# Optimization experiments

Measured on AMD Instinct MI355X. Metric: run time of the kernel, lower is better.

## Reference

```python
import jax, jax.numpy as jnp
import numpy as np

B, T, C, COND, H = 64, 4096, 64, 512, 256
SCALE_EPS = 1e-6
LOGSCALE_FACTOR = 3.0  # glow LinearZeros convention
LEAK = 0.01            # torch LeakyReLU default slope


def setup_inputs() -> dict:
    key = jax.random.key(0)
    ks = jax.random.split(key, 10)
    perm = jnp.asarray(np.random.RandomState(0).permutation(C), dtype=jnp.int32)
    return {
        "input_seq": jax.random.normal(ks[0], (B, T, C), jnp.float32),
        "speech_cond": jax.random.normal(ks[1], (B, T, COND), jnp.float32),
        "actnorm_bias": 0.1 * jax.random.normal(ks[2], (C,), jnp.float32),
        "actnorm_logs": 0.1 * jax.random.normal(ks[3], (C,), jnp.float32),
        "perm": perm,
        "W1": jax.random.normal(ks[4], (C // 2 + COND, H), jnp.float32) / np.sqrt(C // 2 + COND),
        "b1": 0.01 * jax.random.normal(ks[5], (H,), jnp.float32),
        "W2": 0.05 * jax.random.normal(ks[6], (H, C), jnp.float32) / np.sqrt(H),
        "b2": 0.01 * jax.random.normal(ks[7], (C,), jnp.float32),
        "logs2": 0.05 * jax.random.normal(ks[8], (C,), jnp.float32),
    }


def reference(input_seq, speech_cond, actnorm_bias, actnorm_logs, perm, W1, b1, W2, b2, logs2):
    # The torch module loops over timesteps, but each step is independent
    # (no RNN state is used), so we batch all timesteps at once.
    # --- ActNorm2d (per-channel affine); pixels=1 per timestep ---
    z = (input_seq + actnorm_bias) * jnp.exp(actnorm_logs)          # [B,T,C]
    logdet = jnp.full((B,), T * jnp.sum(actnorm_logs))              # [B]
    # --- Permute2d (fixed shuffle of channels) ---
    z = z[..., perm]
    # --- split coupling ---
    z1, z2 = z[..., : C // 2], z[..., C // 2 :]                     # [B,T,C/2] each
    # f_seq: Linear + LeakyReLU (dropout off at eval) + LinearZeros
    h = jnp.concatenate([z1, speech_cond], axis=-1)                 # [B,T,C/2+COND]
    h = jax.nn.leaky_relu(jnp.einsum("btk,kh->bth", h, W1) + b1, LEAK)
    h = (jnp.einsum("bth,hc->btc", h, W2) + b2) * jnp.exp(logs2 * LOGSCALE_FACTOR)  # [B,T,C]
    # --- affine transform: split 'cross' (interleaved) ---
    shift = h[..., 0::2]
    scale = jnp.maximum(jax.nn.sigmoid(h[..., 1::2] + 2.0), SCALE_EPS)
    z2 = (z2 + shift) * scale
    logdet = logdet + jnp.sum(jnp.log(scale), axis=(1, 2))          # [B]
    z_seq = jnp.concatenate([z1, z2], axis=-1)                      # [B,T,C]
    return z_seq, logdet
```

## Files before the change

### kernel.cpp

```cpp
#include <hip/hip_runtime.h>
#include <stdint.h>

#define B_ 64
#define T_ 4096
#define C_ 64
#define COND_ 512
#define H_ 256

typedef __attribute__((ext_vector_type(8))) short short8;
typedef __attribute__((ext_vector_type(4))) float f32x4;
typedef __attribute__((ext_vector_type(2))) float f32x2;
typedef __attribute__((ext_vector_type(2))) unsigned int u32x2;

__device__ __forceinline__ unsigned short f2bf(float x) {
  union { float f; unsigned u; } v; v.f = x;
  unsigned r = v.u + 0x7FFFu + ((v.u >> 16) & 1u);
  return (unsigned short)(r >> 16);
}

__device__ __forceinline__ short8 cvt8(f32x4 lo, f32x4 hi) {
  short8 t;
  t[0] = (short)f2bf(lo[0]); t[1] = (short)f2bf(lo[1]);
  t[2] = (short)f2bf(lo[2]); t[3] = (short)f2bf(lo[3]);
  t[4] = (short)f2bf(hi[0]); t[5] = (short)f2bf(hi[1]);
  t[6] = (short)f2bf(hi[2]); t[7] = (short)f2bf(hi[3]);
  return t;
}

__device__ __forceinline__ void lgkm_barrier() {
  asm volatile("s_waitcnt lgkmcnt(0)" ::: "memory");
  __builtin_amdgcn_s_barrier();
}

#define WS_W1   0
#define WS_W2   278528
#define WS_PB   311296
#define WS_PS   311552
#define WS_B2S  311808

__global__ __launch_bounds__(256) void prep_kernel(
    const float* __restrict__ W1, const float* __restrict__ W2,
    const float* __restrict__ anb, const float* __restrict__ anl,
    const int* __restrict__ perm, const float* __restrict__ b2,
    const float* __restrict__ logs2,
    unsigned short* __restrict__ wsW1, unsigned short* __restrict__ wsW2,
    float* __restrict__ pb, float* __restrict__ ps, float* __restrict__ b2s,
    float* __restrict__ out_ld)
{
  int id = blockIdx.x * 256 + threadIdx.x;
  if (id < 544 * 256) {
    int feat = id & 255, k = id >> 8;
    int r = (k < 512) ? (k + 32) : (k - 512);
    float v = W1[r * 256 + feat];
    int s = k >> 5, MI = feat >> 4;
    int l = (feat & 15) + 16 * ((k >> 3) & 3), i = k & 7;
    wsW1[((s * 16 + MI) * 64 + l) * 8 + i] = f2bf(v);
  } else if (id < 544 * 256 + 256 * 64) {
    int id2 = id - 544 * 256;
    int ch = id2 & 63, k = id2 >> 6;
    float v = W2[k * 64 + ch] * expf(logs2[ch] * 3.0f);
    int s2 = k >> 5, MI2 = ch >> 4;
    int l = (ch & 15) + 16 * ((k >> 3) & 3), i = k & 7;
    wsW2[((s2 * 4 + MI2) * 64 + l) * 8 + i] = f2bf(v);
  } else {
    int c = id - (544 * 256 + 256 * 64);
    if (c < 64) {
      int p = perm[c];
      pb[c] = anb[p];
      ps[c] = expf(anl[p]);
    } else if (c < 128) {
      int ch = c - 64;
      b2s[ch] = b2[ch] * expf(logs2[ch] * 3.0f);
    } else if (c < 192) {
      int b = c - 128;
      float s = 0.f;
      for (int j = 0; j < 64; ++j) s += anl[j];
      out_ld[b] = (float)T_ * s;
    }
  }
}

__global__ __launch_bounds__(256) void flow_main(
    const float* __restrict__ input, const float* __restrict__ cond,
    const int* __restrict__ perm, const float* __restrict__ b1,
    const unsigned short* __restrict__ wsW1, const unsigned short* __restrict__ wsW2,
    const float* __restrict__ pb, const float* __restrict__ ps,
    const float* __restrict__ b2s,
    float* __restrict__ out, float* __restrict__ out_ld)
{
  __shared__ union SM {
    short lA[2][64 * 64];
    short lHT[64 * 256];
  } sm;

  const int tid = threadIdx.x;
  const int w  = tid >> 6;
  const int l  = tid & 63;
  const int lr = l & 15;
  const int lh = l >> 4;
  const long long m0 = (long long)blockIdx.x * 64;

  const int stok = tid >> 2;
  const int skc  = (tid & 3) * 16;
  const float* cpS = cond + (m0 + stok) * 512 + skc;

#define W1F(s, mi) (*(const short8*)&wsW1[((((s) * 16) + (4 * w + (mi))) * 64 + l) * 8])

  short8 aZ[4];
#pragma unroll
  for (int mi = 0; mi < 4; ++mi) aZ[mi] = W1F(16, mi);

  short8 afA[2][4], afB[2][4];
#pragma unroll
  for (int h = 0; h < 2; ++h)
#pragma unroll
    for (int mi = 0; mi < 4; ++mi) afA[h][mi] = W1F(h, mi);
  f32x4 sA0 = *(const f32x4*)(cpS);
  f32x4 sA1 = *(const f32x4*)(cpS + 4);
  f32x4 sA2 = *(const f32x4*)(cpS + 8);
  f32x4 sA3 = *(const f32x4*)(cpS + 12);

#pragma unroll
  for (int h = 0; h < 2; ++h)
#pragma unroll
    for (int mi = 0; mi < 4; ++mi) afB[h][mi] = W1F(2 + h, mi);
  f32x4 sB0 = *(const f32x4*)(cpS + 64);
  f32x4 sB1 = *(const f32x4*)(cpS + 68);
  f32x4 sB2 = *(const f32x4*)(cpS + 72);
  f32x4 sB3 = *(const f32x4*)(cpS + 76);

  {
    const int c0 = (tid & 3) * 8;
    const float* ip = input + (m0 + stok) * 64;
    short8 v;
#pragma unroll
    for (int j = 0; j < 8; ++j) {
      int c = c0 + j;
      v[j] = (short)f2bf((ip[perm[c]] + pb[c]) * ps[c]);
    }
    const int S = (tid & 3) ^ (stok & 7);
    *(short8*)&sm.lA[0][stok * 64 + S * 8] = v;
  }

  f32x4 acc[4][4];
#pragma unroll
  for (int mi = 0; mi < 4; ++mi)
#pragma unroll
    for (int nj = 0; nj < 4; ++nj)
      acc[mi][nj] = (f32x4)0.0f;

  lgkm_barrier();

  {
    short8 bz[4];
#pragma unroll
    for (int nj = 0; nj < 4; ++nj) {
      const int tok = 16 * nj + lr;
      bz[nj] = *(const short8*)&sm.lA[0][tok * 64 + ((lh ^ (tok & 7)) * 8)];
    }
#pragma unroll
    for (int mi = 0; mi < 4; ++mi)
#pragma unroll
      for (int nj = 0; nj < 4; ++nj)
        acc[mi][nj] = __builtin_amdgcn_mfma_f32_16x16x32_bf16(
            aZ[mi], bz[nj], acc[mi][nj], 0, 0, 0);

    short8 c0v = cvt8(sA0, sA1), c1v = cvt8(sA2, sA3);
    const int S0 = 2 * (tid & 3);
    *(short8*)&sm.lA[1][stok * 64 + ((S0 ^ (stok & 7)) * 8)] = c0v;
    *(short8*)&sm.lA[1][stok * 64 + (((S0 + 1) ^ (stok & 7)) * 8)] = c1v;
  }
  lgkm_barrier();

#pragma unroll 1
  for (int p = 0; p < 4; ++p) {
    {
      short8 bf0[4], bf1[4];
#pragma unroll
      for (int nj = 0; nj < 4; ++nj) {
        const int tok = 16 * nj + lr;
        bf0[nj] = *(const short8*)&sm.lA[1][tok * 64 + ((lh ^ (tok & 7)) * 8)];
        bf1[nj] = *(const short8*)&sm.lA[1][tok * 64 + (((4 + lh) ^ (tok & 7)) * 8)];
      }
#pragma unroll
      for (int mi = 0; mi < 4; ++mi)
#pragma unroll
        for (int nj = 0; nj < 4; ++nj)
          acc[mi][nj] = __builtin_amdgcn_mfma_f32_16x16x32_bf16(
              afA[0][mi], bf0[nj], acc[mi][nj], 0, 0, 0);
#pragma unroll
      for (int mi = 0; mi < 4; ++mi)
#pragma unroll
        for (int nj = 0; nj < 4; ++nj)
          acc[mi][nj] = __builtin_amdgcn_mfma_f32_16x16x32_bf16(
              afA[1][mi], bf1[nj], acc[mi][nj], 0, 0, 0);
    }
    if (p <= 2) {
#pragma unroll
      for (int h = 0; h < 2; ++h)
#pragma unroll
        for (int mi = 0; mi < 4; ++mi) afA[h][mi] = W1F(4 * p + 4 + h, mi);
      const float* cp = cpS + (2 * p + 2) * 64;
      sA0 = *(const f32x4*)(cp);
      sA1 = *(const f32x4*)(cp + 4);
      sA2 = *(const f32x4*)(cp + 8);
      sA3 = *(const f32x4*)(cp + 12);
    }
    {
      short8 c0v = cvt8(sB0, sB1), c1v = cvt8(sB2, sB3);
      const int S0 = 2 * (tid & 3);
      *(short8*)&sm.lA[0][stok * 64 + ((S0 ^ (stok & 7)) * 8)] = c0v;
      *(short8*)&sm.lA[0][stok * 64 + (((S0 + 1) ^ (stok & 7)) * 8)] = c1v;
    }
    lgkm_barrier();

    {
      short8 bf0[4], bf1[4];
#pragma unroll
      for (int nj = 0; nj < 4; ++nj) {
        const int tok = 16 * nj + lr;
        bf0[nj] = *(const short8*)&sm.lA[0][tok * 64 + ((lh ^ (tok & 7)) * 8)];
        bf1[nj] = *(const short8*)&sm.lA[0][tok * 64 + (((4 + lh) ^ (tok & 7)) * 8)];
      }
#pragma unroll
      for (int mi = 0; mi < 4; ++mi)
#pragma unroll
        for (int nj = 0; nj < 4; ++nj)
          acc[mi][nj] = __builtin_amdgcn_mfma_f32_16x16x32_bf16(
              afB[0][mi], bf0[nj], acc[mi][nj], 0, 0, 0);
#pragma unroll
      for (int mi = 0; mi < 4; ++mi)
#pragma unroll
        for (int nj = 0; nj < 4; ++nj)
          acc[mi][nj] = __builtin_amdgcn_mfma_f32_16x16x32_bf16(
              afB[1][mi], bf1[nj], acc[mi][nj], 0, 0, 0);
    }
    if (p <= 2) {
#pragma unroll
      for (int h = 0; h < 2; ++h)
#pragma unroll
        for (int mi = 0; mi < 4; ++mi) afB[h][mi] = W1F(4 * p + 6 + h, mi);
      const float* cp = cpS + (2 * p + 3) * 64;
      sB0 = *(const f32x4*)(cp);
      sB1 = *(const f32x4*)(cp + 4);
      sB2 = *(const f32x4*)(cp + 8);
      sB3 = *(const f32x4*)(cp + 12);
    }
    if (p <= 2) {
      short8 c0v = cvt8(sA0, sA1), c1v = cvt8(sA2, sA3);
      const int S0 = 2 * (tid & 3);
      *(short8*)&sm.lA[1][stok * 64 + ((S0 ^ (stok & 7)) * 8)] = c0v;
      *(short8*)&sm.lA[1][stok * 64 + (((S0 + 1) ^ (stok & 7)) * 8)] = c1v;
    }
    lgkm_barrier();
  }

#pragma unroll
  for (int mi = 0; mi < 4; ++mi) {
    const int f0 = 64 * w + 16 * mi + 4 * lh;
    const f32x4 b1v = *(const f32x4*)&b1[f0];
#pragma unroll
    for (int nj = 0; nj < 4; ++nj) {
      const int tok = 16 * nj + lr;
      f32x4 v = acc[mi][nj];
      float h0 = v[0] + b1v[0]; h0 = h0 > 0.f ? h0 : 0.01f * h0;
      float h1 = v[1] + b1v[1]; h1 = h1 > 0.f ? h1 : 0.01f * h1;
      float h2 = v[2] + b1v[2]; h2 = h2 > 0.f ? h2 : 0.01f * h2;
      float h3 = v[3] + b1v[3]; h3 = h3 > 0.f ? h3 : 0.01f * h3;
      u32x2 pk;
      pk[0] = (unsigned)f2bf(h0) | ((unsigned)f2bf(h1) << 16);
      pk[1] = (unsigned)f2bf(h2) | ((unsigned)f2bf(h3) << 16);
      const int off = (tok * 512 + f0 * 2) ^ ((tok & 7) << 4);
      *(u32x2*)((char*)sm.lHT + off) = pk;
    }
  }

  short8 a2r[8];
#pragma unroll
  for (int s2 = 0; s2 < 8; ++s2)
    a2r[s2] = *(const short8*)&wsW2[((s2 * 4 + w) * 64 + l) * 8];

  lgkm_barrier();

  f32x4 acc2[4];
#pragma unroll
  for (int nj = 0; nj < 4; ++nj) acc2[nj] = (f32x4)0.0f;

#pragma unroll
  for (int s2 = 0; s2 < 8; ++s2) {
#pragma unroll
    for (int nj = 0; nj < 4; ++nj) {
      const int tok = 16 * nj + lr;
      const int off = (tok * 512 + (32 * s2 + 8 * lh) * 2) ^ ((tok & 7) << 4);
      const short8 hb = *(const short8*)((char*)sm.lHT + off);
      acc2[nj] = __builtin_amdgcn_mfma_f32_16x16x32_bf16(a2r[s2], hb, acc2[nj], 0, 0, 0);
    }
  }

  const int j0 = 8 * w + 2 * lh;
  const int pA = perm[j0],      pB = perm[j0 + 1];
  const int pC = perm[32 + j0], pD = perm[33 + j0];
  const float bA = pb[j0],      sA = ps[j0];
  const float bB = pb[j0 + 1],  sB = ps[j0 + 1];
  const float bC = pb[32 + j0], sC = ps[32 + j0];
  const float bD = pb[33 + j0], sD = ps[33 + j0];
  const f32x4 b2v = *(const f32x4*)&b2s[16 * w + 4 * lh];

  float ldp = 0.f;
#pragma unroll
  for (int nj = 0; nj < 4; ++nj) {
    const long long row = m0 + 16 * nj + lr;
    const float* ip = input + row * 64;
    float* op = out + row * 64;
    f32x4 v = acc2[nj];
    const float sh0 = v[0] + b2v[0];
    const float sc0 = v[1] + b2v[1];
    const float sh1 = v[2] + b2v[2];
    const float sc1 = v[3] + b2v[3];
    const float scl0 = fmaxf(1.f / (1.f + expf(-(sc0 + 2.f))), 1e-6f);
    const float scl1 = fmaxf(1.f / (1.f + expf(-(sc1 + 2.f))), 1e-6f);
    f32x2 z1o, z2o;
    z1o[0] = (ip[pA] + bA) * sA;
    z1o[1] = (ip[pB] + bB) * sB;
    z2o[0] = ((ip[pC] + bC) * sC + sh0) * scl0;
    z2o[1] = ((ip[pD] + bD) * sD + sh1) * scl1;
    *(f32x2*)(op + j0) = z1o;
    *(f32x2*)(op + 32 + j0) = z2o;
    ldp += logf(scl0) + logf(scl1);
  }

#pragma unroll
  for (int off = 32; off > 0; off >>= 1) ldp += __shfl_xor(ldp, off, 64);
  if (l == 0) atomicAdd(&out_ld[blockIdx.x >> 6], ldp);
}

extern "C" void kernel_launch(void* const* d_in, const int* in_sizes, int n_in,
                              void* d_out, int out_size, void* d_ws, size_t ws_size,
                              hipStream_t stream)
{
  const float* input = (const float*)d_in[0];
  const float* cond  = (const float*)d_in[1];
  const float* anb   = (const float*)d_in[2];
  const float* anl   = (const float*)d_in[3];
  const int*   perm  = (const int*)d_in[4];
  const float* W1    = (const float*)d_in[5];
  const float* b1    = (const float*)d_in[6];
  const float* W2    = (const float*)d_in[7];
  const float* b2    = (const float*)d_in[8];
  const float* logs2 = (const float*)d_in[9];

  float* out    = (float*)d_out;
  float* out_ld = out + (long long)B_ * T_ * C_;

  char* ws = (char*)d_ws;
  unsigned short* wsW1 = (unsigned short*)(ws + WS_W1);
  unsigned short* wsW2 = (unsigned short*)(ws + WS_W2);
  float* pbp  = (float*)(ws + WS_PB);
  float* psp  = (float*)(ws + WS_PS);
  float* b2sp = (float*)(ws + WS_B2S);

  prep_kernel<<<609, 256, 0, stream>>>(W1, W2, anb, anl, perm, b2, logs2,
                                       wsW1, wsW2, pbp, psp, b2sp, out_ld);
  flow_main<<<4096, 256, 0, stream>>>(input, cond, perm, b1, wsW1, wsW2,
                                      pbp, psp, b2sp, out, out_ld);
}
```

Measured before the change: 263.3 us.

## Make flow_main persistent with cross-tile prefetch of input and cond

Launches a fixed grid of 1024 blocks that loop over the 4096 token tiles in a grid-stride fashion, hoisting per-thread permutation and actnorm parameters out of the loop. While the second GEMM and epilogue of one tile run, the next tile's input and first cond slices are loaded into registers. The aim is to hide the global-load latency at tile start and to amortise setup work. The cost is higher register pressure and fewer resident blocks, which may reduce occupancy-based latency hiding. The log-determinant also changes from logf(a)+logf(b) to logf(a*b).

```diff
diff --git a/kernel.cpp b/kernel.cpp
--- a/kernel.cpp
+++ b/kernel.cpp
@@ -6,6 +6,8 @@
 #define C_ 64
 #define COND_ 512
 #define H_ 256
+#define NTILE 4096
+#define GRID_ 1024
 
 typedef __attribute__((ext_vector_type(8))) short short8;
 typedef __attribute__((ext_vector_type(4))) float f32x4;
@@ -98,240 +100,266 @@
   const int l  = tid & 63;
   const int lr = l & 15;
   const int lh = l >> 4;
-  const long long m0 = (long long)blockIdx.x * 64;
 
   const int stok = tid >> 2;
   const int skc  = (tid & 3) * 16;
-  const float* cpS = cond + (m0 + stok) * 512 + skc;
+  const int c0   = (tid & 3) * 8;
 
 #define W1F(s, mi) (*(const short8*)&wsW1[((((s) * 16) + (4 * w + (mi))) * 64 + l) * 8])
 
-  short8 aZ[4];
-#pragma unroll
-  for (int mi = 0; mi < 4; ++mi) aZ[mi] = W1F(16, mi);
-
-  short8 afA[2][4], afB[2][4];
-#pragma unroll
-  for (int h = 0; h < 2; ++h)
-#pragma unroll
-    for (int mi = 0; mi < 4; ++mi) afA[h][mi] = W1F(h, mi);
-  f32x4 sA0 = *(const f32x4*)(cpS);
-  f32x4 sA1 = *(const f32x4*)(cpS + 4);
-  f32x4 sA2 = *(const f32x4*)(cpS + 8);
-  f32x4 sA3 = *(const f32x4*)(cpS + 12);
-
-#pragma unroll
-  for (int h = 0; h < 2; ++h)
-#pragma unroll
-    for (int mi = 0; mi < 4; ++mi) afB[h][mi] = W1F(2 + h, mi);
-  f32x4 sB0 = *(const f32x4*)(cpS + 64);
-  f32x4 sB1 = *(const f32x4*)(cpS + 68);
-  f32x4 sB2 = *(const f32x4*)(cpS + 72);
-  f32x4 sB3 = *(const f32x4*)(cpS + 76);
-
+  int   ipoff[8]; float pbz[8], psz[8];
+#pragma unroll
+  for (int j = 0; j < 8; ++j) {
+    int c = c0 + j;
+    ipoff[j] = perm[c];
+    pbz[j] = pb[c];
+    psz[j] = ps[c];
+  }
+  const int j0 = 8 * w + 2 * lh;
+  const int pi0 = perm[j0],      pi1 = perm[j0 + 1];
+  const int pi2 = perm[32 + j0], pi3 = perm[33 + j0];
+  const float eb0 = pb[j0],      es0 = ps[j0];
+  const float eb1 = pb[j0 + 1],  es1 = ps[j0 + 1];
+  const float eb2 = pb[32 + j0], es2 = ps[32 + j0];
+  const float eb3 = pb[33 + j0], es3 = ps[33 + j0];
+  const f32x4 b2v = *(const f32x4*)&b2s[16 * w + 4 * lh];
+
+  int tile = blockIdx.x;
+  float z1g[8];
+  f32x4 sA0, sA1, sA2, sA3, sB0, sB1, sB2, sB3;
   {
-    const int c0 = (tid & 3) * 8;
-    const float* ip = input + (m0 + stok) * 64;
-    short8 v;
-#pragma unroll
-    for (int j = 0; j < 8; ++j) {
-      int c = c0 + j;
-      v[j] = (short)f2bf((ip[perm[c]] + pb[c]) * ps[c]);
-    }
-    const int S = (tid & 3) ^ (stok & 7);
-    *(short8*)&sm.lA[0][stok * 64 + S * 8] = v;
+    const float* ipn = input + ((long long)tile * 64 + stok) * 64;
+#pragma unroll
+    for (int j = 0; j < 8; ++j) z1g[j] = ipn[ipoff[j]];
+    const float* cpn = cond + ((long long)tile * 64 + stok) * 512 + skc;
+    sA0 = *(const f32x4*)(cpn);      sA1 = *(const f32x4*)(cpn + 4);
+    sA2 = *(const f32x4*)(cpn + 8);  sA3 = *(const f32x4*)(cpn + 12);
+    sB0 = *(const f32x4*)(cpn + 64); sB1 = *(const f32x4*)(cpn + 68);
+    sB2 = *(const f32x4*)(cpn + 72); sB3 = *(const f32x4*)(cpn + 76);
   }
 
-  f32x4 acc[4][4];
-#pragma unroll
-  for (int mi = 0; mi < 4; ++mi)
-#pragma unroll
-    for (int nj = 0; nj < 4; ++nj)
-      acc[mi][nj] = (f32x4)0.0f;
-
-  lgkm_barrier();
-
-  {
-    short8 bz[4];
-#pragma unroll
-    for (int nj = 0; nj < 4; ++nj) {
-      const int tok = 16 * nj + lr;
-      bz[nj] = *(const short8*)&sm.lA[0][tok * 64 + ((lh ^ (tok & 7)) * 8)];
-    }
+#pragma unroll 1
+  for (; tile < NTILE; tile += GRID_) {
+    const long long m0 = (long long)tile * 64;
+    const float* cpS = cond + (m0 + stok) * 512 + skc;
+
+    short8 aZ[4], afA[2][4], afB[2][4];
+#pragma unroll
+    for (int mi = 0; mi < 4; ++mi) aZ[mi] = W1F(16, mi);
+#pragma unroll
+    for (int h = 0; h < 2; ++h)
+#pragma unroll
+      for (int mi = 0; mi < 4; ++mi) afA[h][mi] = W1F(h, mi);
+#pragma unroll
+    for (int h = 0; h < 2; ++h)
+#pragma unroll
+      for (int mi = 0; mi < 4; ++mi) afB[h][mi] = W1F(2 + h, mi);
+
+    lgkm_barrier();
+
+    {
+      short8 v;
+#pragma unroll
+      for (int j = 0; j < 8; ++j)
+        v[j] = (short)f2bf((z1g[j] + pbz[j]) * psz[j]);
+      const int S = (tid & 3) ^ (stok & 7);
+      *(short8*)&sm.lA[0][stok * 64 + S * 8] = v;
+    }
+
+    f32x4 acc[4][4];
 #pragma unroll
     for (int mi = 0; mi < 4; ++mi)
 #pragma unroll
       for (int nj = 0; nj < 4; ++nj)
-        acc[mi][nj] = __builtin_amdgcn_mfma_f32_16x16x32_bf16(
-            aZ[mi], bz[nj], acc[mi][nj], 0, 0, 0);
-
-    short8 c0v = cvt8(sA0, sA1), c1v = cvt8(sA2, sA3);
-    const int S0 = 2 * (tid & 3);
-    *(short8*)&sm.lA[1][stok * 64 + ((S0 ^ (stok & 7)) * 8)] = c0v;
-    *(short8*)&sm.lA[1][stok * 64 + (((S0 + 1) ^ (stok & 7)) * 8)] = c1v;
-  }
-  lgkm_barrier();
-
-#pragma unroll 1
-  for (int p = 0; p < 4; ++p) {
+        acc[mi][nj] = (f32x4)0.0f;
+
+    lgkm_barrier();
+
     {
-      short8 bf0[4], bf1[4];
+      short8 bz[4];
 #pragma unroll
       for (int nj = 0; nj < 4; ++nj) {
         const int tok = 16 * nj + lr;
-        bf0[nj] = *(const short8*)&sm.lA[1][tok * 64 + ((lh ^ (tok & 7)) * 8)];
-        bf1[nj] = *(const short8*)&sm.lA[1][tok * 64 + (((4 + lh) ^ (tok & 7)) * 8)];
+        bz[nj] = *(const short8*)&sm.lA[0][tok * 64 + ((lh ^ (tok & 7)) * 8)];
       }
 #pragma unroll
       for (int mi = 0; mi < 4; ++mi)
 #pragma unroll
         for (int nj = 0; nj < 4; ++nj)
           acc[mi][nj] = __builtin_amdgcn_mfma_f32_16x16x32_bf16(
-              afA[0][mi], bf0[nj], acc[mi][nj], 0, 0, 0);
-#pragma unroll
-      for (int mi = 0; mi < 4; ++mi)
-#pragma unroll
-        for (int nj = 0; nj < 4; ++nj)
-          acc[mi][nj] = __builtin_amdgcn_mfma_f32_16x16x32_bf16(
-              afA[1][mi], bf1[nj], acc[mi][nj], 0, 0, 0);
-    }
-    if (p <= 2) {
-#pragma unroll
-      for (int h = 0; h < 2; ++h)
-#pragma unroll
-        for (int mi = 0; mi < 4; ++mi) afA[h][mi] = W1F(4 * p + 4 + h, mi);
-      const float* cp = cpS + (2 * p + 2) * 64;
-      sA0 = *(const f32x4*)(cp);
-      sA1 = *(const f32x4*)(cp + 4);
-      sA2 = *(const f32x4*)(cp + 8);
-      sA3 = *(const f32x4*)(cp + 12);
-    }
-    {
-      short8 c0v = cvt8(sB0, sB1), c1v = cvt8(sB2, sB3);
-      const int S0 = 2 * (tid & 3);
-      *(short8*)&sm.lA[0][stok * 64 + ((S0 ^ (stok & 7)) * 8)] = c0v;
-      *(short8*)&sm.lA[0][stok * 64 + (((S0 + 1) ^ (stok & 7)) * 8)] = c1v;
-    }
-    lgkm_barrier();
-
-    {
-      short8 bf0[4], bf1[4];
-#pragma unroll
-      for (int nj = 0; nj < 4; ++nj) {
-        const int tok = 16 * nj + lr;
-        bf0[nj] = *(const short8*)&sm.lA[0][tok * 64 + ((lh ^ (tok & 7)) * 8)];
-        bf1[nj] = *(const short8*)&sm.lA[0][tok * 64 + (((4 + lh) ^ (tok & 7)) * 8)];
-      }
-#pragma unroll
-      for (int mi = 0; mi < 4; ++mi)
-#pragma unroll
-        for (int nj = 0; nj < 4; ++nj)
-          acc[mi][nj] = __builtin_amdgcn_mfma_f32_16x16x32_bf16(
-              afB[0][mi], bf0[nj], acc[mi][nj], 0, 0, 0);
-#pragma unroll
-      for (int mi = 0; mi < 4; ++mi)
-#pragma unroll
-        for (int nj = 0; nj < 4; ++nj)
-          acc[mi][nj] = __builtin_amdgcn_mfma_f32_16x16x32_bf16(
-              afB[1][mi], bf1[nj], acc[mi][nj], 0, 0, 0);
-    }
-    if (p <= 2) {
-#pragma unroll
-      for (int h = 0; h < 2; ++h)
-#pragma unroll
-        for (int mi = 0; mi < 4; ++mi) afB[h][mi] = W1F(4 * p + 6 + h, mi);
-      const float* cp = cpS + (2 * p + 3) * 64;
-      sB0 = *(const f32x4*)(cp);
-      sB1 = *(const f32x4*)(cp + 4);
-      sB2 = *(const f32x4*)(cp + 8);
-      sB3 = *(const f32x4*)(cp + 12);
-    }
-    if (p <= 2) {
+              aZ[mi], bz[nj], acc[mi][nj], 0, 0, 0);
+
       short8 c0v = cvt8(sA0, sA1), c1v = cvt8(sA2, sA3);
       const int S0 = 2 * (tid & 3);
       *(short8*)&sm.lA[1][stok * 64 + ((S0 ^ (stok & 7)) * 8)] = c0v;
       *(short8*)&sm.lA[1][stok * 64 + (((S0 + 1) ^ (stok & 7)) * 8)] = c1v;
     }
     lgkm_barrier();
+
+#pragma unroll 1
+    for (int p = 0; p < 4; ++p) {
+      {
+        short8 bf0[4], bf1[4];
+#pragma unroll
+        for (int nj = 0; nj < 4; ++nj) {
+          const int tok = 16 * nj + lr;
+          bf0[nj] = *(const short8*)&sm.lA[1][tok * 64 + ((lh ^ (tok & 7)) * 8)];
+          bf1[nj] = *(const short8*)&sm.lA[1][tok * 64 + (((4 + lh) ^ (tok & 7)) * 8)];
+        }
+#pragma unroll
+        for (int mi = 0; mi < 4; ++mi)
+#pragma unroll
+          for (int nj = 0; nj < 4; ++nj)
+            acc[mi][nj] = __builtin_amdgcn_mfma_f32_16x16x32_bf16(
+                afA[0][mi], bf0[nj], acc[mi][nj], 0, 0, 0);
+#pragma unroll
+        for (int mi = 0; mi < 4; ++mi)
+#pragma unroll
+          for (int nj = 0; nj < 4; ++nj)
+            acc[mi][nj] = __builtin_amdgcn_mfma_f32_16x16x32_bf16(
+                afA[1][mi], bf1[nj], acc[mi][nj], 0, 0, 0);
+      }
+      if (p <= 2) {
+#pragma unroll
+        for (int h = 0; h < 2; ++h)
+#pragma unroll
+          for (int mi = 0; mi < 4; ++mi) afA[h][mi] = W1F(4 * p + 4 + h, mi);
+        const float* cp = cpS + (2 * p + 2) * 64;
+        sA0 = *(const f32x4*)(cp);
+        sA1 = *(const f32x4*)(cp + 4);
+        sA2 = *(const f32x4*)(cp + 8);
+        sA3 = *(const f32x4*)(cp + 12);
+      }
+      {
+        short8 c0v = cvt8(sB0, sB1), c1v = cvt8(sB2, sB3);
+        const int S0 = 2 * (tid & 3);
+        *(short8*)&sm.lA[0][stok * 64 + ((S0 ^ (stok & 7)) * 8)] = c0v;
+        *(short8*)&sm.lA[0][stok * 64 + (((S0 + 1) ^ (stok & 7)) * 8)] = c1v;
+      }
+      lgkm_barrier();
+
+      {
+        short8 bf0[4], bf1[4];
+#pragma unroll
+        for (int nj = 0; nj < 4; ++nj) {
+          const int tok = 16 * nj + lr;
+          bf0[nj] = *(const short8*)&sm.lA[0][tok * 64 + ((lh ^ (tok & 7)) * 8)];
+          bf1[nj] = *(const short8*)&sm.lA[0][tok * 64 + (((4 + lh) ^ (tok & 7)) * 8)];
+        }
+#pragma unroll
+        for (int mi = 0; mi < 4; ++mi)
+#pragma unroll
+          for (int nj = 0; nj < 4; ++nj)
+            acc[mi][nj] = __builtin_amdgcn_mfma_f32_16x16x32_bf16(
+                afB[0][mi], bf0[nj], acc[mi][nj], 0, 0, 0);
+#pragma unroll
+        for (int mi = 0; mi < 4; ++mi)
+#pragma unroll
+          for (int nj = 0; nj < 4; ++nj)
+            acc[mi][nj] = __builtin_amdgcn_mfma_f32_16x16x32_bf16(
+                afB[1][mi], bf1[nj], acc[mi][nj], 0, 0, 0);
+      }
+      if (p <= 2) {
+#pragma unroll
+        for (int h = 0; h < 2; ++h)
+#pragma unroll
+          for (int mi = 0; mi < 4; ++mi) afB[h][mi] = W1F(4 * p + 6 + h, mi);
+        const float* cp = cpS + (2 * p + 3) * 64;
+        sB0 = *(const f32x4*)(cp);
+        sB1 = *(const f32x4*)(cp + 4);
+        sB2 = *(const f32x4*)(cp + 8);
+        sB3 = *(const f32x4*)(cp + 12);
+      }
+      if (p <= 2) {
+        short8 c0v = cvt8(sA0, sA1), c1v = cvt8(sA2, sA3);
+        const int S0 = 2 * (tid & 3);
+        *(short8*)&sm.lA[1][stok * 64 + ((S0 ^ (stok & 7)) * 8)] = c0v;
+        *(short8*)&sm.lA[1][stok * 64 + (((S0 + 1) ^ (stok & 7)) * 8)] = c1v;
+      }
+      lgkm_barrier();
+    }
+
+    short8 a2r[8];
+#pragma unroll
+    for (int s2 = 0; s2 < 8; ++s2)
+      a2r[s2] = *(const short8*)&wsW2[((s2 * 4 + w) * 64 + l) * 8];
+
+    const int ntile = tile + GRID_;
+    if (ntile < NTILE) {
+      const float* ipn = input + ((long long)ntile * 64 + stok) * 64;
+#pragma unroll
+      for (int j = 0; j < 8; ++j) z1g[j] = ipn[ipoff[j]];
+      const float* cpn = cond + ((long long)ntile * 64 + stok) * 512 + skc;
+      sA0 = *(const f32x4*)(cpn);      sA1 = *(const f32x4*)(cpn + 4);
+      sA2 = *(const f32x4*)(cpn + 8);  sA3 = *(const f32x4*)(cpn + 12);
+      sB0 = *(const f32x4*)(cpn + 64); sB1 = *(const f32x4*)(cpn + 68);
+      sB2 = *(const f32x4*)(cpn + 72); sB3 = *(const f32x4*)(cpn + 76);
+    }
+
+#pragma unroll
+    for (int mi = 0; mi < 4; ++mi) {
+      const int f0 = 64 * w + 16 * mi + 4 * lh;
+      const f32x4 b1v = *(const f32x4*)&b1[f0];
+#pragma unroll
+      for (int nj = 0; nj < 4; ++nj) {
+        const int tok = 16 * nj + lr;
+        f32x4 v = acc[mi][nj];
+        float h0 = v[0] + b1v[0]; h0 = h0 > 0.f ? h0 : 0.01f * h0;
+        float h1 = v[1] + b1v[1]; h1 = h1 > 0.f ? h1 : 0.01f * h1;
+        float h2 = v[2] + b1v[2]; h2 = h2 > 0.f ? h2 : 0.01f * h2;
+        float h3 = v[3] + b1v[3]; h3 = h3 > 0.f ? h3 : 0.01f * h3;
+        u32x2 pk;
+        pk[0] = (unsigned)f2bf(h0) | ((unsigned)f2bf(h1) << 16);
+        pk[1] = (unsigned)f2bf(h2) | ((unsigned)f2bf(h3) << 16);
+        const int off = (tok * 512 + f0 * 2) ^ ((tok & 7) << 4);
+        *(u32x2*)((char*)sm.lHT + off) = pk;
+      }
+    }
+
+    lgkm_barrier();
+
+    f32x4 acc2[4];
+#pragma unroll
+    for (int nj = 0; nj < 4; ++nj) acc2[nj] = (f32x4)0.0f;
+
+#pragma unroll
+    for (int s2 = 0; s2 < 8; ++s2) {
+#pragma unroll
+      for (int nj = 0; nj < 4; ++nj) {
+        const int tok = 16 * nj + lr;
+        const int off = (tok * 512 + (32 * s2 + 8 * lh) * 2) ^ ((tok & 7) << 4);
+        const short8 hb = *(const short8*)((char*)sm.lHT + off);
+        acc2[nj] = __builtin_amdgcn_mfma_f32_16x16x32_bf16(a2r[s2], hb, acc2[nj], 0, 0, 0);
+      }
+    }
+
+    float ldp = 0.f;
+#pragma unroll
+    for (int nj = 0; nj < 4; ++nj) {
+      const long long row = m0 + 16 * nj + lr;
+      const float* ip = input + row * 64;
+      float* op = out + row * 64;
+      f32x4 v = acc2[nj];
+      const float sh0 = v[0] + b2v[0];
+      const float sc0 = v[1] + b2v[1];
+      const float sh1 = v[2] + b2v[2];
+      const float sc1 = v[3] + b2v[3];
+      const float scl0 = fmaxf(1.f / (1.f + expf(-(sc0 + 2.f))), 1e-6f);
+      const float scl1 = fmaxf(1.f / (1.f + expf(-(sc1 + 2.f))), 1e-6f);
+      f32x2 z1o, z2o;
+      z1o[0] = (ip[pi0] + eb0) * es0;
+      z1o[1] = (ip[pi1] + eb1) * es1;
+      z2o[0] = ((ip[pi2] + eb2) * es2 + sh0) * scl0;
+      z2o[1] = ((ip[pi3] + eb3) * es3 + sh1) * scl1;
+      *(f32x2*)(op + j0) = z1o;
+      *(f32x2*)(op + 32 + j0) = z2o;
+      ldp += logf(scl0 * scl1);
+    }
+
+#pragma unroll
+    for (int off = 32; off > 0; off >>= 1) ldp += __shfl_xor(ldp, off, 64);
+    if (l == 0) atomicAdd(&out_ld[tile >> 6], ldp);
   }
-
-#pragma unroll
-  for (int mi = 0; mi < 4; ++mi) {
-    const int f0 = 64 * w + 16 * mi + 4 * lh;
-    const f32x4 b1v = *(const f32x4*)&b1[f0];
-#pragma unroll
-    for (int nj = 0; nj < 4; ++nj) {
-      const int tok = 16 * nj + lr;
-      f32x4 v = acc[mi][nj];
-      float h0 = v[0] + b1v[0]; h0 = h0 > 0.f ? h0 : 0.01f * h0;
-      float h1 = v[1] + b1v[1]; h1 = h1 > 0.f ? h1 : 0.01f * h1;
-      float h2 = v[2] + b1v[2]; h2 = h2 > 0.f ? h2 : 0.01f * h2;
-      float h3 = v[3] + b1v[3]; h3 = h3 > 0.f ? h3 : 0.01f * h3;
-      u32x2 pk;
-      pk[0] = (unsigned)f2bf(h0) | ((unsigned)f2bf(h1) << 16);
-      pk[1] = (unsigned)f2bf(h2) | ((unsigned)f2bf(h3) << 16);
-      const int off = (tok * 512 + f0 * 2) ^ ((tok & 7) << 4);
-      *(u32x2*)((char*)sm.lHT + off) = pk;
-    }
-  }
-
-  short8 a2r[8];
-#pragma unroll
-  for (int s2 = 0; s2 < 8; ++s2)
-    a2r[s2] = *(const short8*)&wsW2[((s2 * 4 + w) * 64 + l) * 8];
-
-  lgkm_barrier();
-
-  f32x4 acc2[4];
-#pragma unroll
-  for (int nj = 0; nj < 4; ++nj) acc2[nj] = (f32x4)0.0f;
-
-#pragma unroll
-  for (int s2 = 0; s2 < 8; ++s2) {
-#pragma unroll
-    for (int nj = 0; nj < 4; ++nj) {
-      const int tok = 16 * nj + lr;
-      const int off = (tok * 512 + (32 * s2 + 8 * lh) * 2) ^ ((tok & 7) << 4);
-      const short8 hb = *(const short8*)((char*)sm.lHT + off);
-      acc2[nj] = __builtin_amdgcn_mfma_f32_16x16x32_bf16(a2r[s2], hb, acc2[nj], 0, 0, 0);
-    }
-  }
-
-  const int j0 = 8 * w + 2 * lh;
-  const int pA = perm[j0],      pB = perm[j0 + 1];
-  const int pC = perm[32 + j0], pD = perm[33 + j0];
-  const float bA = pb[j0],      sA = ps[j0];
-  const float bB = pb[j0 + 1],  sB = ps[j0 + 1];
-  const float bC = pb[32 + j0], sC = ps[32 + j0];
-  const float bD = pb[33 + j0], sD = ps[33 + j0];
-  const f32x4 b2v = *(const f32x4*)&b2s[16 * w + 4 * lh];
-
-  float ldp = 0.f;
-#pragma unroll
-  for (int nj = 0; nj < 4; ++nj) {
-    const long long row = m0 + 16 * nj + lr;
-    const float* ip = input + row * 64;
-    float* op = out + row * 64;
-    f32x4 v = acc2[nj];
-    const float sh0 = v[0] + b2v[0];
-    const float sc0 = v[1] + b2v[1];
-    const float sh1 = v[2] + b2v[2];
-    const float sc1 = v[3] + b2v[3];
-    const float scl0 = fmaxf(1.f / (1.f + expf(-(sc0 + 2.f))), 1e-6f);
-    const float scl1 = fmaxf(1.f / (1.f + expf(-(sc1 + 2.f))), 1e-6f);
-    f32x2 z1o, z2o;
-    z1o[0] = (ip[pA] + bA) * sA;
-    z1o[1] = (ip[pB] + bB) * sB;
-    z2o[0] = ((ip[pC] + bC) * sC + sh0) * scl0;
-    z2o[1] = ((ip[pD] + bD) * sD + sh1) * scl1;
-    *(f32x2*)(op + j0) = z1o;
-    *(f32x2*)(op + 32 + j0) = z2o;
-    ldp += logf(scl0) + logf(scl1);
-  }
-
-#pragma unroll
-  for (int off = 32; off > 0; off >>= 1) ldp += __shfl_xor(ldp, off, 64);
-  if (l == 0) atomicAdd(&out_ld[blockIdx.x >> 6], ldp);
 }
 
 extern "C" void kernel_launch(void* const* d_in, const int* in_sizes, int n_in,
@@ -361,6 +389,6 @@
 
   prep_kernel<<<609, 256, 0, stream>>>(W1, W2, anb, anl, perm, b2, logs2,
                                        wsW1, wsW2, pbp, psp, b2sp, out_ld);
-  flow_main<<<4096, 256, 0, stream>>>(input, cond, perm, b1, wsW1, wsW2,
-                                      pbp, psp, b2sp, out, out_ld);
-}
+  flow_main<<<GRID_, 256, 0, stream>>>(input, cond, perm, b1, wsW1, wsW2,
+                                       pbp, psp, b2sp, out, out_ld);
+}
```

Measured after the change: 320.9 us. +21.9%, slower.
